# Performance work log

Measured on AMD Instinct MI355X. Metric: run time of the kernel, lower is better.

The kernel has to match this reference:

```python
import jax, jax.numpy as jnp
import numpy as np
from jax import lax

B, C, L, N = 64, 64, 8192, 3
F = L // 2 + 1  # rfft bins = 4097
HID = 2 * C     # CnnEncoder ratio=2 -> 128
K = 3           # conv kernel size


def setup_inputs() -> dict:
    key = jax.random.key(0)
    ks = jax.random.split(key, 10)
    inp = {
        "x": jax.random.normal(ks[0], (B, C, L), dtype=jnp.float32),
        # spectral filter bank: [N, C, F, 2] (real/imag stacked)
        "parameter": jax.random.normal(ks[1], (N, C, F, 2), dtype=jnp.float32),
        # reweight_R CnnEncoder params (PyTorch Conv1d layout: [out, in, k])
        "wR1": jax.random.normal(ks[2], (HID, C, K), dtype=jnp.float32) * 0.05,
        "bR1": jnp.zeros((HID,), dtype=jnp.float32),
        "wR2": jax.random.normal(ks[3], (N, HID, K), dtype=jnp.float32) * 0.05,
        "bR2": jnp.zeros((N,), dtype=jnp.float32),
        # reweight_I CnnEncoder params
        "wI1": jax.random.normal(ks[4], (HID, C, K), dtype=jnp.float32) * 0.05,
        "bI1": jnp.zeros((HID,), dtype=jnp.float32),
        "wI2": jax.random.normal(ks[5], (N, HID, K), dtype=jnp.float32) * 0.05,
        "bI2": jnp.zeros((N,), dtype=jnp.float32),
    }
    return inp


def _conv1d_same(x, w, b):
    # x: [B, Cin, L]; w: [Cout, Cin, K]; SAME padding for odd K
    pad = (w.shape[-1] - 1) // 2
    y = lax.conv_general_dilated(
        x, w, window_strides=(1,), padding=[(pad, pad)],
        dimension_numbers=("NCH", "OIH", "NCH"))
    return y + b[None, :, None]


def _cnn_encoder(x, w1, b1, w2, b2):
    # conv -> SELU -> (dropout=identity in eval) -> conv -> global avg pool -> softmax over channels
    y = jax.nn.selu(_conv1d_same(x, w1, b1))
    y = _conv1d_same(y, w2, b2)
    y = jnp.mean(y, axis=-1)          # AdaptiveAvgPool1d(1) + squeeze -> [B, N]
    return jax.nn.softmax(y, axis=1)


def reference(x, parameter, wR1, bR1, wR2, bR2, wI1, bI1, wI2, bI2):
    fx = jnp.fft.rfft(x, axis=-1, norm="ortho")          # [B, C, F] complex
    W_R = parameter[..., 0]                               # [N, C, F]
    W_I = parameter[..., 1]
    C_R = _cnn_encoder(fx.real, wR1, bR1, wR2, bR2)       # [B, N]
    C_I = _cnn_encoder(fx.imag, wI1, bI1, wI2, bI2)       # [B, N]
    Kf_R = jnp.einsum("bn,ncf->bcf", C_R, W_R)            # [B, C, F]
    Kf_I = jnp.einsum("bn,ncf->bcf", C_I, W_I)
    Kf = lax.complex(Kf_R, Kf_I)
    out = jnp.fft.irfft(fx * Kf, n=L, axis=-1, norm="ortho")  # [B, C, L]
    return out
```

## Files before the change

kernel.cpp:

```cpp
#include <hip/hip_runtime.h>
#include <math.h>

#define BB 64
#define CCH 64
#define LL 8192
#define FF 4097
#define FP 4104
#define M4 4096
#define NT 65

typedef __attribute__((ext_vector_type(8))) short short8;
typedef __attribute__((ext_vector_type(4))) float floatx4;

__device__ __forceinline__ short f2bf(float v) {
    union { float f; unsigned u; } cv; cv.f = v;
    unsigned r = (cv.u + 0x7fffu + ((cv.u >> 16) & 1u)) >> 16;
    return (short)r;
}

__device__ __forceinline__ float2 cadd(float2 a, float2 b){ return make_float2(a.x+b.x, a.y+b.y); }
__device__ __forceinline__ float2 csub(float2 a, float2 b){ return make_float2(a.x-b.x, a.y-b.y); }
__device__ __forceinline__ float2 cmul(float2 a, float2 b){ return make_float2(a.x*b.x-a.y*b.y, a.x*b.y+a.y*b.x); }
template<int SIGN> __device__ __forceinline__ float2 roti(float2 a){
    return (SIGN < 0) ? make_float2(a.y, -a.x) : make_float2(-a.y, a.x);
}
template<int SIGN>
__device__ __forceinline__ void dft4(float2& a, float2& b, float2& c, float2& d){
    float2 t0 = cadd(a,c), t1 = csub(a,c), t2 = cadd(b,d), t3 = roti<SIGN>(csub(b,d));
    a = cadd(t0,t2); b = cadd(t1,t3); c = csub(t0,t2); d = csub(t1,t3);
}

template<int SIGN>
__device__ __forceinline__ void dft16(float2 v[16]){
    const float C1 = 0.9238795325112867f, S1 = 0.3826834323650898f, R2 = 0.7071067811865476f;
    const float sg = (SIGN < 0) ? -1.0f : 1.0f;
#pragma unroll
    for (int n1 = 0; n1 < 4; ++n1) dft4<SIGN>(v[n1], v[n1+4], v[n1+8], v[n1+12]);
    const float2 W1 = make_float2( C1, sg*S1);
    const float2 W2 = make_float2( R2, sg*R2);
    const float2 W3 = make_float2( S1, sg*C1);
    const float2 W6 = make_float2(-R2, sg*R2);
    const float2 W9 = make_float2(-C1, -sg*S1);
    v[5]  = cmul(v[5],  W1); v[6]  = cmul(v[6],  W2); v[7]  = cmul(v[7],  W3);
    v[9]  = cmul(v[9],  W2); v[10] = roti<SIGN>(v[10]); v[11] = cmul(v[11], W6);
    v[13] = cmul(v[13], W3); v[14] = cmul(v[14], W6); v[15] = cmul(v[15], W9);
#pragma unroll
    for (int k2 = 0; k2 < 4; ++k2) dft4<SIGN>(v[4*k2+0], v[4*k2+1], v[4*k2+2], v[4*k2+3]);
    float2 t[16];
#pragma unroll
    for (int k = 0; k < 16; ++k) t[k] = v[4*(k & 3) + (k >> 2)];
#pragma unroll
    for (int k = 0; k < 16; ++k) v[k] = t[k];
}

__device__ __forceinline__ void twiddle_pow(float2 v[16], float ang){
    float s, c; __sincosf(ang, &s, &c);
    float2 w = make_float2(c, s), t = w;
    v[1] = cmul(v[1], t);
#pragma unroll
    for (int j = 2; j < 16; ++j){ t = cmul(t, w); v[j] = cmul(v[j], t); }
}

template<int SIGN>
__device__ __forceinline__ void fft4096_regs(float2 v[16], float2* lds, int tid){
    const float TWO_PI = 6.283185307179586f;
    const float sg = (SIGN < 0) ? -1.0f : 1.0f;
    int n1 = tid & 15, hi = tid >> 4;
    dft16<SIGN>(v);
    twiddle_pow(v, sg * TWO_PI * (float)hi * (1.0f/256.0f));
#pragma unroll
    for (int j = 0; j < 16; ++j) lds[j*256 + tid] = v[j];
    __syncthreads();
#pragma unroll
    for (int j = 0; j < 16; ++j) v[j] = lds[hi*256 + j*16 + n1];
    __syncthreads();
    dft16<SIGN>(v);
#pragma unroll
    for (int j = 0; j < 16; ++j) lds[(j*16 + hi)*16 + (n1 ^ hi)] = v[j];
    __syncthreads();
#pragma unroll
    for (int j = 0; j < 16; ++j) v[j] = lds[tid*16 + (j ^ n1)];
    twiddle_pow(v, sg * TWO_PI * (float)tid * (1.0f/4096.0f));
    dft16<SIGN>(v);
    __syncthreads();
}

#define COSJ_INIT { 1.0f, 0.980785280403230f, 0.923879532511287f, 0.831469612302545f, \
    0.707106781186548f, 0.555570233019602f, 0.382683432365090f, 0.195090322016128f, \
    0.0f, -0.195090322016128f, -0.382683432365090f, -0.555570233019602f, \
    -0.707106781186548f, -0.831469612302545f, -0.923879532511287f, -0.980785280403230f }
#define SINJ_INIT { 0.0f, 0.195090322016128f, 0.382683432365090f, 0.555570233019602f, \
    0.707106781186548f, 0.831469612302545f, 0.923879532511287f, 0.980785280403230f, \
    1.0f, 0.980785280403230f, 0.923879532511287f, 0.831469612302545f, \
    0.707106781186548f, 0.555570233019602f, 0.382683432365090f, 0.195090322016128f }

__global__ __launch_bounds__(256, 5) void k_rfft(const float* __restrict__ x,
                                                 float* __restrict__ fxr,
                                                 float* __restrict__ fxi)
{
    __shared__ float2 lds[4096];
    int bc = blockIdx.x, tid = threadIdx.x;
    const float2* xr = (const float2*)(x + (size_t)bc * LL);
    float2 v[16];
#pragma unroll
    for (int j = 0; j < 16; ++j) v[j] = xr[tid + 256*j];
    fft4096_regs<-1>(v, lds, tid);
#pragma unroll
    for (int j = 0; j < 16; ++j) lds[tid + 256*j] = v[j];
    __syncthreads();

    const float scale = 0.011048543456039806f;
    const float COSJ[16] = COSJ_INIT;
    const float SINJ[16] = SINJ_INIT;
    size_t row = (size_t)bc * FP;
    float sA, cA; __sincosf(3.14159265358979f * (float)tid * (1.0f/4096.0f), &sA, &cA);
#pragma unroll
    for (int j = 0; j < 16; ++j){
        int k = tid + 256*j;
        if (k == 0){
            float2 z0 = lds[0];
            fxr[row + 0]  = (z0.x + z0.y) * scale; fxi[row + 0]  = 0.0f;
            fxr[row + M4] = (z0.x - z0.y) * scale; fxi[row + M4] = 0.0f;
        } else {
            float2 zk = lds[k], zm = lds[(4096 - k) & 4095];
            float er = 0.5f*(zk.x + zm.x), ei = 0.5f*(zk.y - zm.y);
            float dr = 0.5f*(zk.x - zm.x), di = 0.5f*(zk.y + zm.y);
            float cp = cA*COSJ[j] - sA*SINJ[j];
            float sp = sA*COSJ[j] + cA*SINJ[j];
            fxr[row + k] = (er + cp*di - sp*dr) * scale;
            fxi[row + k] = (ei - cp*dr - sp*di) * scale;
        }
    }
}

__global__ __launch_bounds__(256) void k_pack(const float* __restrict__ wR1,
                                              const float* __restrict__ wI1,
                                              short* __restrict__ Wp)
{
    int idx = blockIdx.x * 256 + threadIdx.x;
    if (idx >= 2 * 128 * 192) return;
    int enc = idx / (128 * 192);
    int rem = idx - enc * (128 * 192);
    int h = rem / 192;
    int k = rem - h * 192;
    int s = k >> 5;
    int j = k & 31;
    int kap = s >> 1;
    int c = (s & 1) * 32 + j;
    const float* w = enc ? wI1 : wR1;
    Wp[idx] = f2bf(w[(h * 64 + c) * 3 + kap]);
}

__global__ __launch_bounds__(256, 5) void k_conv_mfma(const float* __restrict__ fxr,
                                                      const float* __restrict__ fxi,
                                                      const short* __restrict__ Wp,
                                                      const float* __restrict__ bR1,
                                                      const float* __restrict__ bI1,
                                                      float* __restrict__ part,
                                                      float* __restrict__ e0,
                                                      float* __restrict__ e1)
{
    __shared__ short Xt[66 * 64];
    int tile = blockIdx.x;
    int b    = blockIdx.y;
    int enc  = blockIdx.z;
    const float* src = enc ? fxi : fxr;
    const float* b1  = enc ? bI1 : bR1;
    int tid = threadIdx.x;
    int t0 = tile * 64;
    const float* xb = src + (size_t)b * 64 * FP;

    int w = tid >> 6;
    int lane = tid & 63;
    int n = lane & 15;
    int q = lane >> 4;
    int h0 = w * 32;

    short8 afrag[2][6];
    const short* wbase = Wp + (size_t)enc * 128 * 192;
#pragma unroll
    for (int hb = 0; hb < 2; ++hb)
#pragma unroll
        for (int s = 0; s < 6; ++s)
            afrag[hb][s] = *(const short8*)(wbase + (h0 + hb * 16 + n) * 192 + s * 32 + q * 8);

    float4 b1q[2];
#pragma unroll
    for (int hb = 0; hb < 2; ++hb)
        b1q[hb] = *(const float4*)(b1 + h0 + hb * 16 + q * 4);

    int sw  = tid >> 6;
    int scc = tid & 63;
    {
        const float* srow = xb + (size_t)scc * FP + t0 + sw * 16;
        float4 f0 = *(const float4*)(srow + 0);
        float4 f1 = *(const float4*)(srow + 4);
        float4 f2 = *(const float4*)(srow + 8);
        float4 f3 = *(const float4*)(srow + 12);
        float vals[16] = { f0.x, f0.y, f0.z, f0.w,  f1.x, f1.y, f1.z, f1.w,
                           f2.x, f2.y, f2.z, f2.w,  f3.x, f3.y, f3.z, f3.w };
        bool allv = (t0 + 64) <= FF;
#pragma unroll
        for (int u = 0; u < 16; ++u) {
            float val = vals[u];
            if (!allv) val = (t0 + sw * 16 + u) < FF ? val : 0.0f;
            int tt = sw * 16 + u + 1;
            Xt[(tt * 64 + scc) ^ ((tt & 7) << 3)] = f2bf(val);
        }
        if (tid < 128) {
            int hhal = tid >> 6;
            int ht = hhal ? (t0 + 64) : (t0 - 1);
            int hts = ht < 0 ? 0 : (ht >= FF ? FF - 1 : ht);
            float v = xb[(size_t)scc * FP + hts];
            if (ht < 0 || ht >= FF) v = 0.0f;
            int tt = hhal ? 65 : 0;
            Xt[(tt * 64 + scc) ^ ((tt & 7) << 3)] = f2bf(v);
        }
    }

#pragma unroll
    for (int hb = 0; hb < 2; ++hb)
#pragma unroll
        for (int s = 0; s < 6; ++s)
            asm volatile("" :: "v"(afrag[hb][s]));

    __syncthreads();

    floatx4 acc[2][4];
#pragma unroll
    for (int hb = 0; hb < 2; ++hb)
#pragma unroll
        for (int tb = 0; tb < 4; ++tb) {
            acc[hb][tb][0] = b1q[hb].x;
            acc[hb][tb][1] = b1q[hb].y;
            acc[hb][tb][2] = b1q[hb].z;
            acc[hb][tb][3] = b1q[hb].w;
        }

#pragma unroll
    for (int s = 0; s < 6; ++s) {
        int kap = s >> 1;
        int cbase = (s & 1) * 32 + q * 8;
#pragma unroll
        for (int tb = 0; tb < 4; ++tb) {
            int row = tb * 16 + n + kap;
            short8 bfrag = *(const short8*)(Xt + ((row * 64 + cbase) ^ ((row & 7) << 3)));
            acc[0][tb] = __builtin_amdgcn_mfma_f32_16x16x32_bf16(afrag[0][s], bfrag, acc[0][tb], 0, 0, 0);
            acc[1][tb] = __builtin_amdgcn_mfma_f32_16x16x32_bf16(afrag[1][s], bfrag, acc[1][tb], 0, 0, 0);
        }
    }

    const float SELU_S = 1.0507009873554805f;
    const float SELU_A = 1.6732632423543772f;
    int ebase = (enc * 64 + b) * 128;
    bool edge = (t0 == 0) || (t0 == 4096);
    bool allv = (t0 + 63) < FF;
    float hsum[2][4] = {{0.f,0.f,0.f,0.f},{0.f,0.f,0.f,0.f}};
#pragma unroll
    for (int hb = 0; hb < 2; ++hb) {
#pragma unroll
        for (int tb = 0; tb < 4; ++tb) {
            int t = t0 + tb * 16 + n;
            bool valid = t < FF;
#pragma unroll
            for (int r = 0; r < 4; ++r) {
                float val = acc[hb][tb][r];
                float y = SELU_S * (val > 0.0f ? val : SELU_A * (__expf(val) - 1.0f));
                if (!allv) y = valid ? y : 0.0f;
                hsum[hb][r] += y;
                if (edge) {
                    int h = h0 + hb * 16 + q * 4 + r;
                    if (t == 0)      e0[ebase + h] = y;
                    if (t == FF - 1) e1[ebase + h] = y;
                }
            }
        }
    }

#pragma unroll
    for (int off = 1; off < 16; off <<= 1)
#pragma unroll
        for (int hb = 0; hb < 2; ++hb)
#pragma unroll
            for (int r = 0; r < 4; ++r)
                hsum[hb][r] += __shfl_xor(hsum[hb][r], off, 64);

    if (n == 0) {
#pragma unroll
        for (int hb = 0; hb < 2; ++hb) {
            size_t idx = ((size_t)(tile * 2 + enc) * 64 + b) * 128 + h0 + hb * 16 + q * 4;
            *(float4*)(part + idx) = make_float4(hsum[hb][0], hsum[hb][1], hsum[hb][2], hsum[hb][3]);
        }
    }
}

__global__ __launch_bounds__(128) void k_head(const float* __restrict__ part,
                                              const float* __restrict__ e0,
                                              const float* __restrict__ e1,
                                              const float* __restrict__ wR2,
                                              const float* __restrict__ bR2,
                                              const float* __restrict__ wI2,
                                              const float* __restrict__ bI2,
                                              float* __restrict__ Cw)
{
    __shared__ float red[3][128];
    int b   = blockIdx.x;
    int enc = blockIdx.y;
    const float* w2 = enc ? wI2 : wR2;
    const float* b2 = enc ? bI2 : bR2;
    int h = threadIdx.x;
    float T = 0.0f;
    for (int t = 0; t < NT; ++t)
        T += part[((size_t)(t * 2 + enc) * 64 + b) * 128 + h];
    float e0v = e0[(enc * 64 + b) * 128 + h];
    float e1v = e1[(enc * 64 + b) * 128 + h];
#pragma unroll
    for (int nn = 0; nn < 3; ++nn) {
        const float* wp = w2 + (nn * 128 + h) * 3;
        red[nn][h] = wp[0] * (T - e1v) + wp[1] * T + wp[2] * (T - e0v);
    }
    __syncthreads();
    if (h < 64) {
        float lg[3];
#pragma unroll
        for (int nn = 0; nn < 3; ++nn) {
            float s = red[nn][h] + red[nn][h + 64];
#pragma unroll
            for (int off = 1; off < 64; off <<= 1)
                s += __shfl_xor(s, off, 64);
            lg[nn] = b2[nn] + s / 4097.0f;
        }
        if (h == 0) {
            float mx = fmaxf(lg[0], fmaxf(lg[1], lg[2]));
            float ex0 = __expf(lg[0] - mx);
            float ex1 = __expf(lg[1] - mx);
            float ex2 = __expf(lg[2] - mx);
            float den = ex0 + ex1 + ex2;
            Cw[(enc * 64 + b) * 3 + 0] = ex0 / den;
            Cw[(enc * 64 + b) * 3 + 1] = ex1 / den;
            Cw[(enc * 64 + b) * 3 + 2] = ex2 / den;
        }
    }
}

__global__ __launch_bounds__(256, 5) void k_irfft(const float* __restrict__ fxr,
                                                  const float* __restrict__ fxi,
                                                  const float* __restrict__ param,
                                                  const float* __restrict__ Cw,
                                                  float* __restrict__ out)
{
    __shared__ float2 lds[4096];
    int bc = blockIdx.x, b = bc >> 6, c = bc & 63, tid = threadIdx.x;
    float cr0 = Cw[b*3+0], cr1 = Cw[b*3+1], cr2 = Cw[b*3+2];
    float ci0 = Cw[192 + b*3+0], ci1 = Cw[192 + b*3+1], ci2 = Cw[192 + b*3+2];
    size_t row = (size_t)bc * FP;
    const float2* W0 = (const float2*)param + (size_t)(0*64 + c) * FF;
    const float2* W1 = (const float2*)param + (size_t)(1*64 + c) * FF;
    const float2* W2 = (const float2*)param + (size_t)(2*64 + c) * FF;

    for (int f = tid; f < 4096; f += 256) {
        float2 w0 = W0[f], w1 = W1[f], w2 = W2[f];
        float kr = cr0*w0.x + cr1*w1.x + cr2*w2.x;
        float ki = ci0*w0.y + ci1*w1.y + ci2*w2.y;
        float fr = fxr[row + f], fi = fxi[row + f];
        float Pr = fr*kr - fi*ki;
        float Pi = fr*ki + fi*kr;
        if (f == 0) {
            float2 u0 = W0[4096], u1 = W1[4096], u2 = W2[4096];
            float krn = cr0*u0.x + cr1*u1.x + cr2*u2.x;
            Pi = fxr[row + 4096] * krn;
        }
        lds[f] = make_float2(Pr, Pi);
    }
    __syncthreads();

    const float COSJ[16] = COSJ_INIT;
    const float SINJ[16] = SINJ_INIT;
    float2 v[16];
    float sA, cA; __sincosf(3.14159265358979f * (float)tid * (1.0f/4096.0f), &sA, &cA);
#pragma unroll
    for (int j = 0; j < 16; ++j) {
        int m = tid + 256*j;
        if (m == 0) {
            float p0 = lds[0].x, pn = lds[0].y;
            v[j] = make_float2(0.5f*(p0 + pn), 0.5f*(p0 - pn));
        } else {
            float2 p = lds[m], qq = lds[4096 - m];
            float er = 0.5f*(p.x + qq.x), ei = 0.5f*(p.y - qq.y);
            float dr = 0.5f*(p.x - qq.x), di = 0.5f*(p.y + qq.y);
            float cp = cA*COSJ[j] - sA*SINJ[j];
            float sp = sA*COSJ[j] + cA*SINJ[j];
            float zor = dr*cp - di*sp;
            float zoi = dr*sp + di*cp;
            v[j] = make_float2(er - zoi, ei + zor);
        }
    }
    __syncthreads();
    fft4096_regs<1>(v, lds, tid);

    const float S = 0.02209708691207961f;
    float2* orow = (float2*)(out + (size_t)bc * LL);
#pragma unroll
    for (int j = 0; j < 16; ++j) {
        float2 z = v[j];
        orow[tid + 256*j] = make_float2(S*z.x, S*z.y);
    }
}

extern "C" void kernel_launch(void* const* d_in, const int* in_sizes, int n_in,
                              void* d_out, int out_size, void* d_ws, size_t ws_size,
                              hipStream_t stream)
{
    (void)in_sizes; (void)n_in; (void)out_size; (void)ws_size;
    const float* x   = (const float*)d_in[0];
    const float* prm = (const float*)d_in[1];
    const float* wR1 = (const float*)d_in[2];
    const float* bR1 = (const float*)d_in[3];
    const float* wR2 = (const float*)d_in[4];
    const float* bR2 = (const float*)d_in[5];
    const float* wI1 = (const float*)d_in[6];
    const float* bI1 = (const float*)d_in[7];
    const float* wI2 = (const float*)d_in[8];
    const float* bI2 = (const float*)d_in[9];
    float* out = (float*)d_out;
    float* ws  = (float*)d_ws;

    size_t o = 0;
    float* fxr  = ws + o; o += (size_t)BB * CCH * FP;
    float* fxi  = ws + o; o += (size_t)BB * CCH * FP;
    float* part = ws + o; o += (size_t)NT * 2 * 64 * 128;
    float* e0   = ws + o; o += 2 * 64 * 128;
    float* e1   = ws + o; o += 2 * 64 * 128;
    float* Cw   = ws + o; o += 2 * 64 * 4;
    short* Wp   = (short*)(ws + o); o += (size_t)2 * 128 * 192 / 2;

    k_rfft<<<dim3(4096), dim3(256), 0, stream>>>(x, fxr, fxi);
    k_pack<<<dim3((2 * 128 * 192 + 255) / 256), dim3(256), 0, stream>>>(wR1, wI1, Wp);
    k_conv_mfma<<<dim3(NT, 64, 2), dim3(256), 0, stream>>>(fxr, fxi, Wp, bR1, bI1,
                                                           part, e0, e1);
    k_head<<<dim3(64, 2), dim3(128), 0, stream>>>(part, e0, e1, wR2, bR2, wI2, bI2, Cw);
    k_irfft<<<dim3(4096), dim3(256), 0, stream>>>(fxr, fxi, prm, Cw, out);
}
```

Measured before the change: 400.0 us.

## Halve FFT shared memory by exchanging real and imaginary parts separately

The 4096-point FFT transposes and the real-FFT post/pre-processing now go through a 16 KB float LDS buffer instead of a 32 KB float2 buffer. Real and imaginary parts are exchanged in two passes, and the bank swizzle is changed to suit 4-byte elements. This frees shared memory so launch bounds can target 6 blocks per CU instead of 5. In exchange each exchange needs twice as many LDS round trips and barriers, and more live registers.

Measured after the change: 405.3 us. No clear change (+1.3%).

```diff
diff --git a/kernel.cpp b/kernel.cpp
--- a/kernel.cpp
+++ b/kernel.cpp
@@ -62,24 +62,43 @@
 }
 
 template<int SIGN>
-__device__ __forceinline__ void fft4096_regs(float2 v[16], float2* lds, int tid){
+__device__ __forceinline__ void fft4096f(float2 v[16], float* lds, int tid){
     const float TWO_PI = 6.283185307179586f;
     const float sg = (SIGN < 0) ? -1.0f : 1.0f;
     int n1 = tid & 15, hi = tid >> 4;
+    float tr[16];
     dft16<SIGN>(v);
     twiddle_pow(v, sg * TWO_PI * (float)hi * (1.0f/256.0f));
 #pragma unroll
-    for (int j = 0; j < 16; ++j) lds[j*256 + tid] = v[j];
-    __syncthreads();
-#pragma unroll
-    for (int j = 0; j < 16; ++j) v[j] = lds[hi*256 + j*16 + n1];
+    for (int j = 0; j < 16; ++j) lds[j*256 + tid] = v[j].x;
+    __syncthreads();
+#pragma unroll
+    for (int j = 0; j < 16; ++j) tr[j] = lds[hi*256 + j*16 + n1];
+    __syncthreads();
+#pragma unroll
+    for (int j = 0; j < 16; ++j) lds[j*256 + tid] = v[j].y;
+    __syncthreads();
+#pragma unroll
+    for (int j = 0; j < 16; ++j) { v[j].y = lds[hi*256 + j*16 + n1]; v[j].x = tr[j]; }
     __syncthreads();
     dft16<SIGN>(v);
 #pragma unroll
-    for (int j = 0; j < 16; ++j) lds[(j*16 + hi)*16 + (n1 ^ hi)] = v[j];
-    __syncthreads();
-#pragma unroll
-    for (int j = 0; j < 16; ++j) v[j] = lds[tid*16 + (j ^ n1)];
+    for (int j = 0; j < 16; ++j) {
+        int row = j*16 + hi;
+        lds[row*16 + (n1 ^ ((row >> 1) & 15))] = v[j].x;
+    }
+    __syncthreads();
+#pragma unroll
+    for (int j = 0; j < 16; ++j) tr[j] = lds[tid*16 + (j ^ ((tid >> 1) & 15))];
+    __syncthreads();
+#pragma unroll
+    for (int j = 0; j < 16; ++j) {
+        int row = j*16 + hi;
+        lds[row*16 + (n1 ^ ((row >> 1) & 15))] = v[j].y;
+    }
+    __syncthreads();
+#pragma unroll
+    for (int j = 0; j < 16; ++j) { v[j].y = lds[tid*16 + (j ^ ((tid >> 1) & 15))]; v[j].x = tr[j]; }
     twiddle_pow(v, sg * TWO_PI * (float)tid * (1.0f/4096.0f));
     dft16<SIGN>(v);
     __syncthreads();
@@ -94,19 +113,32 @@
     1.0f, 0.980785280403230f, 0.923879532511287f, 0.831469612302545f, \
     0.707106781186548f, 0.555570233019602f, 0.382683432365090f, 0.195090322016128f }
 
-__global__ __launch_bounds__(256, 5) void k_rfft(const float* __restrict__ x,
+__global__ __launch_bounds__(256, 6) void k_rfft(const float* __restrict__ x,
                                                  float* __restrict__ fxr,
                                                  float* __restrict__ fxi)
 {
-    __shared__ float2 lds[4096];
+    __shared__ float lds[4096];
     int bc = blockIdx.x, tid = threadIdx.x;
     const float2* xr = (const float2*)(x + (size_t)bc * LL);
     float2 v[16];
 #pragma unroll
     for (int j = 0; j < 16; ++j) v[j] = xr[tid + 256*j];
-    fft4096_regs<-1>(v, lds, tid);
-#pragma unroll
-    for (int j = 0; j < 16; ++j) lds[tid + 256*j] = v[j];
+    fft4096f<-1>(v, lds, tid);
+
+#pragma unroll
+    for (int j = 0; j < 16; ++j) lds[tid + 256*j] = v[j].x;
+    __syncthreads();
+    float er[16], dr[16];
+#pragma unroll
+    for (int j = 0; j < 16; ++j) {
+        int k = tid + 256*j;
+        float a = lds[k], bq = lds[(4096 - k) & 4095];
+        er[j] = 0.5f*(a + bq);
+        dr[j] = 0.5f*(a - bq);
+    }
+    __syncthreads();
+#pragma unroll
+    for (int j = 0; j < 16; ++j) lds[tid + 256*j] = v[j].y;
     __syncthreads();
 
     const float scale = 0.011048543456039806f;
@@ -117,18 +149,16 @@
 #pragma unroll
     for (int j = 0; j < 16; ++j){
         int k = tid + 256*j;
+        float ay = lds[k], by = lds[(4096 - k) & 4095];
         if (k == 0){
-            float2 z0 = lds[0];
-            fxr[row + 0]  = (z0.x + z0.y) * scale; fxi[row + 0]  = 0.0f;
-            fxr[row + M4] = (z0.x - z0.y) * scale; fxi[row + M4] = 0.0f;
+            fxr[row + 0]  = (er[0] + ay) * scale; fxi[row + 0]  = 0.0f;
+            fxr[row + M4] = (er[0] - ay) * scale; fxi[row + M4] = 0.0f;
         } else {
-            float2 zk = lds[k], zm = lds[(4096 - k) & 4095];
-            float er = 0.5f*(zk.x + zm.x), ei = 0.5f*(zk.y - zm.y);
-            float dr = 0.5f*(zk.x - zm.x), di = 0.5f*(zk.y + zm.y);
+            float ei = 0.5f*(ay - by), di = 0.5f*(ay + by);
             float cp = cA*COSJ[j] - sA*SINJ[j];
             float sp = sA*COSJ[j] + cA*SINJ[j];
-            fxr[row + k] = (er + cp*di - sp*dr) * scale;
-            fxi[row + k] = (ei - cp*dr - sp*di) * scale;
+            fxr[row + k] = (er[j] + cp*di - sp*dr[j]) * scale;
+            fxi[row + k] = (ei - cp*dr[j] - sp*di) * scale;
         }
     }
 }
@@ -343,13 +373,13 @@
     }
 }
 
-__global__ __launch_bounds__(256, 5) void k_irfft(const float* __restrict__ fxr,
+__global__ __launch_bounds__(256, 6) void k_irfft(const float* __restrict__ fxr,
                                                   const float* __restrict__ fxi,
                                                   const float* __restrict__ param,
                                                   const float* __restrict__ Cw,
                                                   float* __restrict__ out)
 {
-    __shared__ float2 lds[4096];
+    __shared__ float lds[4096];
     int bc = blockIdx.x, b = bc >> 6, c = bc & 63, tid = threadIdx.x;
     float cr0 = Cw[b*3+0], cr1 = Cw[b*3+1], cr2 = Cw[b*3+2];
     float ci0 = Cw[192 + b*3+0], ci1 = Cw[192 + b*3+1], ci2 = Cw[192 + b*3+2];
@@ -358,7 +388,10 @@
     const float2* W1 = (const float2*)param + (size_t)(1*64 + c) * FF;
     const float2* W2 = (const float2*)param + (size_t)(2*64 + c) * FF;
 
-    for (int f = tid; f < 4096; f += 256) {
+    float pi_s[16];
+#pragma unroll
+    for (int j = 0; j < 16; ++j) {
+        int f = tid + 256*j;
         float2 w0 = W0[f], w1 = W1[f], w2 = W2[f];
         float kr = cr0*w0.x + cr1*w1.x + cr2*w2.x;
         float ki = ci0*w0.y + ci1*w1.y + ci2*w2.y;
@@ -370,8 +403,22 @@
             float krn = cr0*u0.x + cr1*u1.x + cr2*u2.x;
             Pi = fxr[row + 4096] * krn;
         }
-        lds[f] = make_float2(Pr, Pi);
-    }
+        lds[f] = Pr;
+        pi_s[j] = Pi;
+    }
+    __syncthreads();
+
+    float er[16], dr[16];
+#pragma unroll
+    for (int j = 0; j < 16; ++j) {
+        int m = tid + 256*j;
+        float pr = lds[m], qr = lds[(4096 - m) & 4095];
+        er[j] = 0.5f*(pr + qr);
+        dr[j] = 0.5f*(pr - qr);
+    }
+    __syncthreads();
+#pragma unroll
+    for (int j = 0; j < 16; ++j) lds[tid + 256*j] = pi_s[j];
     __syncthreads();
 
     const float COSJ[16] = COSJ_INIT;
@@ -381,22 +428,21 @@
 #pragma unroll
     for (int j = 0; j < 16; ++j) {
         int m = tid + 256*j;
+        float pi = lds[m], qi = lds[(4096 - m) & 4095];
         if (m == 0) {
-            float p0 = lds[0].x, pn = lds[0].y;
+            float p0 = er[0], pn = pi;
             v[j] = make_float2(0.5f*(p0 + pn), 0.5f*(p0 - pn));
         } else {
-            float2 p = lds[m], qq = lds[4096 - m];
-            float er = 0.5f*(p.x + qq.x), ei = 0.5f*(p.y - qq.y);
-            float dr = 0.5f*(p.x - qq.x), di = 0.5f*(p.y + qq.y);
+            float ei = 0.5f*(pi - qi), di = 0.5f*(pi + qi);
             float cp = cA*COSJ[j] - sA*SINJ[j];
             float sp = sA*COSJ[j] + cA*SINJ[j];
-            float zor = dr*cp - di*sp;
-            float zoi = dr*sp + di*cp;
-            v[j] = make_float2(er - zoi, ei + zor);
-        }
-    }
-    __syncthreads();
-    fft4096_regs<1>(v, lds, tid);
+            float zor = dr[j]*cp - di*sp;
+            float zoi = dr[j]*sp + di*cp;
+            v[j] = make_float2(er[j] - zoi, ei + zor);
+        }
+    }
+    __syncthreads();
+    fft4096f<1>(v, lds, tid);
 
     const float S = 0.02209708691207961f;
     float2* orow = (float2*)(out + (size_t)bc * LL);
```
